# Optimization experiments

Measured on AMD Instinct MI355X. Metric: run time of the kernel, lower is better.

## Reference

```python
import jax, jax.numpy as jnp
import numpy as np

N = 65536          # num nodes
E = N * 16         # num edges (avg degree 16)
F_IN, F_HID, F_OUT = 128, 128, 16


def _xavier(key, shape):
    fan_in, fan_out = shape
    limit = (6.0 / (fan_in + fan_out)) ** 0.5
    return jax.random.uniform(key, shape, jnp.float32, -limit, limit)


def setup_inputs() -> dict:
    key = jax.random.key(0)
    k1, k2, k3, k4, k5 = jax.random.split(key, 5)
    x = jax.random.normal(k1, (N, F_IN), jnp.float32)
    u = jax.random.randint(k2, (E,), 0, N, jnp.int32)  # edge sources (rows of adj)
    v = jax.random.randint(k3, (E,), 0, N, jnp.int32)  # edge targets (cols of adj)
    # symmetric normalization: D = bincount(u); w = D[u]^-0.5 * D[v]^-0.5
    deg = jnp.zeros((N,), jnp.float32).at[u].add(1.0)
    inv_sqrt_d = jnp.where(deg > 0, deg ** -0.5, 0.0)
    edge_weight = inv_sqrt_d[u] * inv_sqrt_d[v]
    W1 = _xavier(k4, (F_IN, F_HID))
    W2 = _xavier(k5, (F_HID, F_OUT))
    return {"x": x, "u": u, "v": v, "edge_weight": edge_weight, "W1": W1, "W2": W2}


def _spmm(u, v, w, x):
    # (adj @ x)[u] = sum over edges (u,v): w * x[v]
    return jax.ops.segment_sum(w[:, None] * x[v], u, num_segments=N)


def reference(x, u, v, edge_weight, W1, W2):
    # layer 1: relu((adj @ x) @ W1)   (dropout is identity in eval mode)
    h = jax.nn.relu(_spmm(u, v, edge_weight, x) @ W1)
    # layer 2: (adj @ h) @ W2
    return _spmm(u, v, edge_weight, h) @ W2
```

## Files before the change

kernel.cpp:

```cpp
#include <hip/hip_runtime.h>

#define NN 65536
#define FH 128
#define FO 16
#define NE (NN * 16)
#define EPB 4096
#define BCAP 8192

typedef unsigned short u16x8 __attribute__((ext_vector_type(8)));
typedef unsigned short u16x4 __attribute__((ext_vector_type(4)));
typedef float f32x4 __attribute__((ext_vector_type(4)));
typedef short s16x8 __attribute__((ext_vector_type(8)));

__device__ inline float b2f(unsigned short u) {
    union { unsigned int i; float f; } x;
    x.i = ((unsigned int)u) << 16;
    return x.f;
}
__device__ inline unsigned short f2bf(float f) {
    union { float f; unsigned int i; } x;
    x.f = f;
    unsigned int r = x.i + 0x7fff + ((x.i >> 16) & 1);
    return (unsigned short)(r >> 16);
}

__global__ __launch_bounds__(256) void w1cvt(const float* __restrict__ W1,
                                             unsigned short* __restrict__ w1t) {
    const int gid = blockIdx.x * 256 + threadIdx.x;
    const int c = gid >> 4;
    const int k0 = (gid & 15) * 8;
    u16x8 o;
#pragma unroll
    for (int j = 0; j < 8; ++j) o[j] = f2bf(W1[(size_t)(k0 + j) * 128 + c]);
    *(u16x8*)&w1t[(size_t)c * 128 + k0] = o;
}

__global__ __launch_bounds__(256) void bucketA(const int* __restrict__ eu,
                                               const int* __restrict__ ev,
                                               unsigned int* __restrict__ tmp,
                                               int* __restrict__ cnts,
                                               int* __restrict__ offs) {
    __shared__ int lhist[256];
    __shared__ int lscan[256];
    __shared__ int lcur[256];
    __shared__ unsigned int lsorted[EPB];
    const int tid = threadIdx.x;
    const int blk = blockIdx.x;
    lhist[tid] = 0;
    __syncthreads();
    const int e0 = blk * EPB;
    int us[16], vs[16];
#pragma unroll
    for (int k = 0; k < 16; ++k) {
        int e = e0 + k * 256 + tid;
        us[k] = eu[e];
        vs[k] = ev[e];
        atomicAdd(&lhist[us[k] >> 8], 1);
    }
    __syncthreads();
    const int c = lhist[tid];
    lscan[tid] = c;
    __syncthreads();
    for (int off = 1; off < 256; off <<= 1) {
        int v = (tid >= off) ? lscan[tid - off] : 0;
        __syncthreads();
        lscan[tid] += v;
        __syncthreads();
    }
    const int start = lscan[tid] - c;
    lcur[tid] = start;
    cnts[blk * 256 + tid] = c;
    offs[blk * 256 + tid] = start;
    __syncthreads();
#pragma unroll
    for (int k = 0; k < 16; ++k) {
        int bin = us[k] >> 8;
        int pos = atomicAdd(&lcur[bin], 1);
        lsorted[pos] = (((unsigned int)(us[k] & 255)) << 16) | (unsigned int)vs[k];
    }
    __syncthreads();
    for (int i = tid; i < EPB; i += 256) {
        tmp[(size_t)blk * EPB + i] = lsorted[i];
    }
}

__global__ __launch_bounds__(256) void bucketB(const unsigned int* __restrict__ tmp,
                                               const int* __restrict__ cnts,
                                               const int* __restrict__ offs,
                                               unsigned short* __restrict__ evw16,
                                               int* __restrict__ row_start,
                                               int* __restrict__ deg,
                                               float* __restrict__ isd) {
    __shared__ int lcnt[256];
    __shared__ int lscan[256];
    __shared__ int lcur[256];
    __shared__ int stot;
    __shared__ unsigned int lrec[BCAP];
    __shared__ unsigned short lbuf[BCAP];
    const int b = blockIdx.x;
    const int tid = threadIdx.x;
    const int ct = cnts[tid * 256 + b];
    const int roff = offs[tid * 256 + b];
    lscan[tid] = ct;
    __syncthreads();
    for (int off = 1; off < 256; off <<= 1) {
        int v = (tid >= off) ? lscan[tid - off] : 0;
        __syncthreads();
        lscan[tid] += v;
        __syncthreads();
    }
    const int rbase = lscan[tid] - ct;
    if (tid == 255) stot = lscan[255];
    __syncthreads();
    const int total = stot;
    const unsigned int* src = &tmp[(size_t)tid * EPB + roff];
    for (int k = 0; k < ct; ++k) lrec[rbase + k] = src[k];
    lcnt[tid] = 0;
    __syncthreads();
    for (int i = tid; i < total; i += 256) {
        atomicAdd(&lcnt[lrec[i] >> 16], 1);
    }
    __syncthreads();
    const int c = lcnt[tid];
    lscan[tid] = c;
    __syncthreads();
    for (int off = 1; off < 256; off <<= 1) {
        int v = (tid >= off) ? lscan[tid - off] : 0;
        __syncthreads();
        lscan[tid] += v;
        __syncthreads();
    }
    const int myStart = lscan[tid] - c;
    lcur[tid] = myStart;
    const int node = b * 256 + tid;
    row_start[node] = b * BCAP + myStart;
    deg[node] = c;
    isd[node] = (c > 0) ? (1.0f / sqrtf((float)c)) : 0.0f;
    __syncthreads();
    for (int i = tid; i < total; i += 256) {
        unsigned int rec = lrec[i];
        int off = atomicAdd(&lcur[rec >> 16], 1);
        lbuf[off] = (unsigned short)(rec & 0xFFFFu);
    }
    __syncthreads();
    for (int i = tid; i < total; i += 256) {
        evw16[(size_t)b * BCAP + i] = lbuf[i];
    }
}

__global__ __launch_bounds__(256) void gemm1_mfma(const float* __restrict__ x,
                                                  const unsigned short* __restrict__ w1t,
                                                  const float* __restrict__ isd,
                                                  unsigned short* __restrict__ t1s) {
    __shared__ unsigned short wsT[128][136];
    const int tid = threadIdx.x;
    const int row0 = blockIdx.x * 64;
    for (int i = tid; i < 2048; i += 256) {
        int cc = i >> 4;
        int k0 = (i & 15) * 8;
        *(u16x8*)&wsT[cc][k0] = *(const u16x8*)&w1t[(size_t)cc * 128 + k0];
    }
    const int lane = tid & 63;
    const int w = tid >> 6;
    const int ar = row0 + w * 16 + (lane & 15);
    const int k0 = (lane >> 4) * 8;
    s16x8 afrag[4];
#pragma unroll
    for (int kk = 0; kk < 4; ++kk) {
        float4 va = *(const float4*)&x[(size_t)ar * 128 + kk * 32 + k0];
        float4 vb = *(const float4*)&x[(size_t)ar * 128 + kk * 32 + k0 + 4];
        u16x8 t;
        t[0] = f2bf(va.x); t[1] = f2bf(va.y); t[2] = f2bf(va.z); t[3] = f2bf(va.w);
        t[4] = f2bf(vb.x); t[5] = f2bf(vb.y); t[6] = f2bf(vb.z); t[7] = f2bf(vb.w);
        afrag[kk] = *(s16x8*)&t;
    }
    __syncthreads();
    f32x4 acc[8];
#pragma unroll
    for (int n = 0; n < 8; ++n) acc[n] = (f32x4){0.f, 0.f, 0.f, 0.f};
#pragma unroll
    for (int n = 0; n < 8; ++n) {
        const int bc = n * 16 + (lane & 15);
#pragma unroll
        for (int kk = 0; kk < 4; ++kk) {
            s16x8 bfrag = *(const s16x8*)&wsT[bc][kk * 32 + k0];
            acc[n] = __builtin_amdgcn_mfma_f32_16x16x32_bf16(afrag[kk], bfrag, acc[n], 0, 0, 0);
        }
    }
    const int orow = row0 + w * 16 + (lane >> 4) * 4;
    const float s0 = isd[orow + 0];
    const float s1 = isd[orow + 1];
    const float s2 = isd[orow + 2];
    const float s3 = isd[orow + 3];
#pragma unroll
    for (int n = 0; n < 8; ++n) {
        const int col = n * 16 + (lane & 15);
        t1s[(size_t)(orow + 0) * 128 + col] = f2bf(s0 * acc[n][0]);
        t1s[(size_t)(orow + 1) * 128 + col] = f2bf(s1 * acc[n][1]);
        t1s[(size_t)(orow + 2) * 128 + col] = f2bf(s2 * acc[n][2]);
        t1s[(size_t)(orow + 3) * 128 + col] = f2bf(s3 * acc[n][3]);
    }
}

__global__ __launch_bounds__(256) void fused_agg_gemm2(const int* __restrict__ row_start,
                                                       const int* __restrict__ deg,
                                                       const unsigned short* __restrict__ evw16,
                                                       const float* __restrict__ isd,
                                                       const unsigned short* __restrict__ src,
                                                       const float* __restrict__ W2,
                                                       unsigned short* __restrict__ t2s) {
    __shared__ unsigned short hs[16][136];
    __shared__ unsigned short w2T[16][136];
    __shared__ unsigned short lidx[1024];
    const int tid = threadIdx.x;
    const int n0 = blockIdx.x * 16;
    const int eb = row_start[n0];
    const int ee = row_start[n0 + 15] + deg[n0 + 15];
    const int cnt = ee - eb;
    for (int i = tid; i < cnt; i += 256) lidx[i] = evw16[eb + i];
    for (int i = tid; i < 128 * 16; i += 256) {
        int k = i >> 4, cc = i & 15;
        w2T[cc][k] = f2bf(W2[i]);
    }
    const int slot = tid >> 4;
    const int node = n0 + slot;
    const int c0 = (tid & 15) * 8;
    const int rs = row_start[node];
    const int d = deg[node];
    const int ib = rs - eb;
    const float s = isd[node];
    __syncthreads();
    float acc[8] = {};
    int p = 0;
    for (; p + 8 <= d; p += 8) {
        int v0 = lidx[ib + p + 0];
        int v1 = lidx[ib + p + 1];
        int v2 = lidx[ib + p + 2];
        int v3 = lidx[ib + p + 3];
        int v4 = lidx[ib + p + 4];
        int v5 = lidx[ib + p + 5];
        int v6 = lidx[ib + p + 6];
        int v7 = lidx[ib + p + 7];
        u16x8 a0 = *(const u16x8*)&src[(size_t)v0 * 128 + c0];
        u16x8 a1 = *(const u16x8*)&src[(size_t)v1 * 128 + c0];
        u16x8 a2 = *(const u16x8*)&src[(size_t)v2 * 128 + c0];
        u16x8 a3 = *(const u16x8*)&src[(size_t)v3 * 128 + c0];
        u16x8 a4 = *(const u16x8*)&src[(size_t)v4 * 128 + c0];
        u16x8 a5 = *(const u16x8*)&src[(size_t)v5 * 128 + c0];
        u16x8 a6 = *(const u16x8*)&src[(size_t)v6 * 128 + c0];
        u16x8 a7 = *(const u16x8*)&src[(size_t)v7 * 128 + c0];
#pragma unroll
        for (int j = 0; j < 8; ++j)
            acc[j] += ((b2f(a0[j]) + b2f(a1[j])) + (b2f(a2[j]) + b2f(a3[j]))) +
                      ((b2f(a4[j]) + b2f(a5[j])) + (b2f(a6[j]) + b2f(a7[j])));
    }
    for (; p + 2 <= d; p += 2) {
        int v0 = lidx[ib + p + 0];
        int v1 = lidx[ib + p + 1];
        u16x8 a0 = *(const u16x8*)&src[(size_t)v0 * 128 + c0];
        u16x8 a1 = *(const u16x8*)&src[(size_t)v1 * 128 + c0];
#pragma unroll
        for (int j = 0; j < 8; ++j) acc[j] += b2f(a0[j]) + b2f(a1[j]);
    }
    if (p < d) {
        int v0 = lidx[ib + p];
        u16x8 a = *(const u16x8*)&src[(size_t)v0 * 128 + c0];
#pragma unroll
        for (int j = 0; j < 8; ++j) acc[j] += b2f(a[j]);
    }
    u16x8 o;
#pragma unroll
    for (int j = 0; j < 8; ++j) o[j] = f2bf(fmaxf(s * acc[j], 0.f));
    *(u16x8*)&hs[slot][c0] = o;
    __syncthreads();
    const int tx = tid & 15;
    float acc2 = 0.f;
#pragma unroll
    for (int k = 0; k < 128; k += 8) {
        u16x8 hv = *(const u16x8*)&hs[slot][k];
        u16x8 wv = *(const u16x8*)&w2T[tx][k];
#pragma unroll
        for (int j = 0; j < 8; ++j) acc2 += b2f(hv[j]) * b2f(wv[j]);
    }
    t2s[(size_t)node * 16 + tx] = f2bf(s * acc2);
}

__global__ __launch_bounds__(256) void spmm_gather16f(const int* __restrict__ row_start,
                                                      const int* __restrict__ deg,
                                                      const unsigned short* __restrict__ evw16,
                                                      const float* __restrict__ isd,
                                                      const unsigned short* __restrict__ t2s,
                                                      float* __restrict__ out) {
    __shared__ unsigned short lidx[2048];
    const int tid = threadIdx.x;
    const int n0 = blockIdx.x * 64;
    const int eb = row_start[n0];
    const int ee = row_start[n0 + 63] + deg[n0 + 63];
    const int cnt = ee - eb;
    for (int i = tid; i < cnt; i += 256) lidx[i] = evw16[eb + i];
    const int node = n0 + (tid >> 2);
    const int j = (tid & 3) * 4;
    const int rs = row_start[node];
    const int d = deg[node];
    const int ib = rs - eb;
    const float s = isd[node];
    __syncthreads();
    float acc0 = 0.f, acc1 = 0.f, acc2 = 0.f, acc3 = 0.f;
    int p = 0;
    for (; p + 4 <= d; p += 4) {
        int v0 = lidx[ib + p + 0];
        int v1 = lidx[ib + p + 1];
        int v2 = lidx[ib + p + 2];
        int v3 = lidx[ib + p + 3];
        u16x4 a0 = *(const u16x4*)&t2s[(size_t)v0 * 16 + j];
        u16x4 a1 = *(const u16x4*)&t2s[(size_t)v1 * 16 + j];
        u16x4 a2 = *(const u16x4*)&t2s[(size_t)v2 * 16 + j];
        u16x4 a3 = *(const u16x4*)&t2s[(size_t)v3 * 16 + j];
        acc0 += (b2f(a0[0]) + b2f(a1[0])) + (b2f(a2[0]) + b2f(a3[0]));
        acc1 += (b2f(a0[1]) + b2f(a1[1])) + (b2f(a2[1]) + b2f(a3[1]));
        acc2 += (b2f(a0[2]) + b2f(a1[2])) + (b2f(a2[2]) + b2f(a3[2]));
        acc3 += (b2f(a0[3]) + b2f(a1[3])) + (b2f(a2[3]) + b2f(a3[3]));
    }
    for (; p < d; ++p) {
        int v = lidx[ib + p];
        u16x4 a = *(const u16x4*)&t2s[(size_t)v * 16 + j];
        acc0 += b2f(a[0]);
        acc1 += b2f(a[1]);
        acc2 += b2f(a[2]);
        acc3 += b2f(a[3]);
    }
    float4 o;
    o.x = s * acc0;
    o.y = s * acc1;
    o.z = s * acc2;
    o.w = s * acc3;
    *(float4*)&out[(size_t)node * 16 + j] = o;
}

extern "C" void kernel_launch(void* const* d_in, const int* in_sizes, int n_in,
                              void* d_out, int out_size, void* d_ws, size_t ws_size,
                              hipStream_t stream) {
    const float* x  = (const float*)d_in[0];
    const int*   eu = (const int*)d_in[1];
    const int*   ev = (const int*)d_in[2];
    const float* W1 = (const float*)d_in[4];
    const float* W2 = (const float*)d_in[5];
    float* out = (float*)d_out;

    char* p = (char*)d_ws;
    int* row_start        = (int*)p;            p += (size_t)NN * 4;
    int* deg              = (int*)p;            p += (size_t)NN * 4;
    float* isd            = (float*)p;          p += (size_t)NN * 4;
    int* cnts             = (int*)p;            p += (size_t)256 * 256 * 4;
    int* offs             = (int*)p;            p += (size_t)256 * 256 * 4;
    unsigned int* tmp     = (unsigned int*)p;   p += (size_t)NE * 4;
    unsigned short* evw16 = (unsigned short*)p; p += (size_t)256 * BCAP * 2;
    unsigned short* w1t   = (unsigned short*)p; p += (size_t)FH * FH * 2;
    unsigned short* t1s   = (unsigned short*)p; p += (size_t)NN * FH * 2;
    unsigned short* t2s   = (unsigned short*)p;

    w1cvt<<<8, 256, 0, stream>>>(W1, w1t);

    bucketA<<<NE / EPB, 256, 0, stream>>>(eu, ev, tmp, cnts, offs);
    bucketB<<<256, 256, 0, stream>>>(tmp, cnts, offs, evw16, row_start, deg, isd);

    gemm1_mfma<<<NN / 64, 256, 0, stream>>>(x, w1t, isd, t1s);

    fused_agg_gemm2<<<NN / 16, 256, 0, stream>>>(row_start, deg, evw16, isd, t1s, W2, t2s);

    spmm_gather16f<<<NN / 64, 256, 0, stream>>>(row_start, deg, evw16, isd, t2s, out);
}
```

Baseline: 86.89 us.

## Fold W1 conversion into bucketA, parallelize bucket gather, unroll final gather by 8

Three changes land together. The W1-to-bf16 transpose kernel becomes eight extra blocks of bucketA, which removes one launch. In bucketB, each thread previously copied its own whole run serially; now all threads copy the bucket cooperatively, finding each element's source run by binary search over the run-end prefix sums, so the global reads are coalesced and the load is balanced. The final 16-wide gather is unrolled from 4 to 8 edges per step to keep more loads in flight, at the cost of more registers.

Measured after the change: 93.53 us. 7.6% more time.

```diff
diff --git a/kernel.cpp b/kernel.cpp
--- a/kernel.cpp
+++ b/kernel.cpp
@@ -24,28 +24,29 @@
     return (unsigned short)(r >> 16);
 }
 
-__global__ __launch_bounds__(256) void w1cvt(const float* __restrict__ W1,
-                                             unsigned short* __restrict__ w1t) {
-    const int gid = blockIdx.x * 256 + threadIdx.x;
-    const int c = gid >> 4;
-    const int k0 = (gid & 15) * 8;
-    u16x8 o;
-#pragma unroll
-    for (int j = 0; j < 8; ++j) o[j] = f2bf(W1[(size_t)(k0 + j) * 128 + c]);
-    *(u16x8*)&w1t[(size_t)c * 128 + k0] = o;
-}
-
 __global__ __launch_bounds__(256) void bucketA(const int* __restrict__ eu,
                                                const int* __restrict__ ev,
                                                unsigned int* __restrict__ tmp,
                                                int* __restrict__ cnts,
-                                               int* __restrict__ offs) {
+                                               int* __restrict__ offs,
+                                               const float* __restrict__ W1,
+                                               unsigned short* __restrict__ w1t) {
+    const int tid = threadIdx.x;
+    const int blk = blockIdx.x;
+    if (blk >= 256) {
+        const int gid = (blk - 256) * 256 + tid;
+        const int c = gid >> 4;
+        const int k0 = (gid & 15) * 8;
+        u16x8 o;
+#pragma unroll
+        for (int j = 0; j < 8; ++j) o[j] = f2bf(W1[(size_t)(k0 + j) * 128 + c]);
+        *(u16x8*)&w1t[(size_t)c * 128 + k0] = o;
+        return;
+    }
     __shared__ int lhist[256];
     __shared__ int lscan[256];
     __shared__ int lcur[256];
     __shared__ unsigned int lsorted[EPB];
-    const int tid = threadIdx.x;
-    const int blk = blockIdx.x;
     lhist[tid] = 0;
     __syncthreads();
     const int e0 = blk * EPB;
@@ -94,6 +95,8 @@
     __shared__ int lcnt[256];
     __shared__ int lscan[256];
     __shared__ int lcur[256];
+    __shared__ int lrunend[256];
+    __shared__ int lgsrc[256];
     __shared__ int stot;
     __shared__ unsigned int lrec[BCAP];
     __shared__ unsigned short lbuf[BCAP];
@@ -109,12 +112,20 @@
         lscan[tid] += v;
         __syncthreads();
     }
-    const int rbase = lscan[tid] - ct;
+    lrunend[tid] = lscan[tid];
+    lgsrc[tid] = tid * EPB + roff;
     if (tid == 255) stot = lscan[255];
     __syncthreads();
     const int total = stot;
-    const unsigned int* src = &tmp[(size_t)tid * EPB + roff];
-    for (int k = 0; k < ct; ++k) lrec[rbase + k] = src[k];
+    for (int i = tid; i < total; i += 256) {
+        int lo = 0, hi = 255;
+        while (lo < hi) {
+            int mid = (lo + hi) >> 1;
+            if (lrunend[mid] > i) hi = mid; else lo = mid + 1;
+        }
+        int rb = (lo == 0) ? 0 : lrunend[lo - 1];
+        lrec[i] = tmp[(size_t)lgsrc[lo] + (i - rb)];
+    }
     lcnt[tid] = 0;
     __syncthreads();
     for (int i = tid; i < total; i += 256) {
@@ -307,23 +318,26 @@
     __syncthreads();
     float acc0 = 0.f, acc1 = 0.f, acc2 = 0.f, acc3 = 0.f;
     int p = 0;
-    for (; p + 4 <= d; p += 4) {
-        int v0 = lidx[ib + p + 0];
-        int v1 = lidx[ib + p + 1];
-        int v2 = lidx[ib + p + 2];
-        int v3 = lidx[ib + p + 3];
-        u16x4 a0 = *(const u16x4*)&t2s[(size_t)v0 * 16 + j];
-        u16x4 a1 = *(const u16x4*)&t2s[(size_t)v1 * 16 + j];
-        u16x4 a2 = *(const u16x4*)&t2s[(size_t)v2 * 16 + j];
-        u16x4 a3 = *(const u16x4*)&t2s[(size_t)v3 * 16 + j];
-        acc0 += (b2f(a0[0]) + b2f(a1[0])) + (b2f(a2[0]) + b2f(a3[0]));
-        acc1 += (b2f(a0[1]) + b2f(a1[1])) + (b2f(a2[1]) + b2f(a3[1]));
-        acc2 += (b2f(a0[2]) + b2f(a1[2])) + (b2f(a2[2]) + b2f(a3[2]));
-        acc3 += (b2f(a0[3]) + b2f(a1[3])) + (b2f(a2[3]) + b2f(a3[3]));
+    for (; p + 8 <= d; p += 8) {
+        u16x4 a0 = *(const u16x4*)&t2s[(size_t)lidx[ib + p + 0] * 16 + j];
+        u16x4 a1 = *(const u16x4*)&t2s[(size_t)lidx[ib + p + 1] * 16 + j];
+        u16x4 a2 = *(const u16x4*)&t2s[(size_t)lidx[ib + p + 2] * 16 + j];
+        u16x4 a3 = *(const u16x4*)&t2s[(size_t)lidx[ib + p + 3] * 16 + j];
+        u16x4 a4 = *(const u16x4*)&t2s[(size_t)lidx[ib + p + 4] * 16 + j];
+        u16x4 a5 = *(const u16x4*)&t2s[(size_t)lidx[ib + p + 5] * 16 + j];
+        u16x4 a6 = *(const u16x4*)&t2s[(size_t)lidx[ib + p + 6] * 16 + j];
+        u16x4 a7 = *(const u16x4*)&t2s[(size_t)lidx[ib + p + 7] * 16 + j];
+        acc0 += ((b2f(a0[0]) + b2f(a1[0])) + (b2f(a2[0]) + b2f(a3[0]))) +
+                ((b2f(a4[0]) + b2f(a5[0])) + (b2f(a6[0]) + b2f(a7[0])));
+        acc1 += ((b2f(a0[1]) + b2f(a1[1])) + (b2f(a2[1]) + b2f(a3[1]))) +
+                ((b2f(a4[1]) + b2f(a5[1])) + (b2f(a6[1]) + b2f(a7[1])));
+        acc2 += ((b2f(a0[2]) + b2f(a1[2])) + (b2f(a2[2]) + b2f(a3[2]))) +
+                ((b2f(a4[2]) + b2f(a5[2])) + (b2f(a6[2]) + b2f(a7[2])));
+        acc3 += ((b2f(a0[3]) + b2f(a1[3])) + (b2f(a2[3]) + b2f(a3[3]))) +
+                ((b2f(a4[3]) + b2f(a5[3])) + (b2f(a6[3]) + b2f(a7[3])));
     }
     for (; p < d; ++p) {
-        int v = lidx[ib + p];
-        u16x4 a = *(const u16x4*)&t2s[(size_t)v * 16 + j];
+        u16x4 a = *(const u16x4*)&t2s[(size_t)lidx[ib + p] * 16 + j];
         acc0 += b2f(a[0]);
         acc1 += b2f(a[1]);
         acc2 += b2f(a[2]);
@@ -359,9 +373,7 @@
     unsigned short* t1s   = (unsigned short*)p; p += (size_t)NN * FH * 2;
     unsigned short* t2s   = (unsigned short*)p;
 
-    w1cvt<<<8, 256, 0, stream>>>(W1, w1t);
-
-    bucketA<<<NE / EPB, 256, 0, stream>>>(eu, ev, tmp, cnts, offs);
+    bucketA<<<NE / EPB + 8, 256, 0, stream>>>(eu, ev, tmp, cnts, offs, W1, w1t);
     bucketB<<<256, 256, 0, stream>>>(tmp, cnts, offs, evw16, row_start, deg, isd);
 
     gemm1_mfma<<<NN / 64, 256, 0, stream>>>(x, w1t, isd, t1s);
```
